# Optimization experiments

Hardware: AMD Instinct MI355X
Metric: run time of the kernel (lower is better)

The kernel has to match this reference:

```python
import jax, jax.numpy as jnp
import numpy as np


def setup_inputs() -> dict:
    key = jax.random.key(0)
    k1, k2 = jax.random.split(key)
    B, M, L, C, F, K = 8, 32, 1024, 256, 256, 3
    x = jax.random.normal(k1, (B, M, L, C), dtype=jnp.float32)
    W = jax.random.normal(k2, (K, C, F), dtype=jnp.float32) * 0.02  # WIO layout
    b = jnp.zeros((F,), dtype=jnp.float32)
    return {"x": x, "W": W, "b": b}


def reference(x, W, b):
    # Original: tf.map_fn(Conv1D, x) over leading axis of [B, M, L, C].
    # Mathematically identical to one batched 'valid' Conv1D on [B*M, L, C].
    B, M, L, C = x.shape
    K, _, F = W.shape
    xf = x.reshape(B * M, L, C)
    y = jax.lax.conv_general_dilated(
        xf, W,
        window_strides=(1,),
        padding='VALID',
        dimension_numbers=('NWC', 'WIO', 'NWC'),
    ) + b
    return y.reshape(B, M, L - K + 1, F)
```

## Files before the change

### kernel.cpp

```cpp
#include <hip/hip_runtime.h>

typedef __attribute__((ext_vector_type(8))) short short8;
typedef __attribute__((ext_vector_type(4))) float f32x4;

constexpr int L = 1024, C = 256, F = 256;
constexpr int NIMG = 256;
constexpr int LOUT = 1022;
constexpr int KTOT = 768;
constexpr int BK = 32;
constexpr int NKI = KTOT / BK;
constexpr int LDT = 40;
constexpr long MAXROW = (long)NIMG * L - 1;

__device__ inline unsigned short f2bf(float f) {
  union { float f; unsigned u; } v; v.f = f;
  return (unsigned short)((v.u + 0x7FFFu + ((v.u >> 16) & 1u)) >> 16);
}

__device__ inline void g2l16(const unsigned short* g, unsigned short* l) {
  __builtin_amdgcn_global_load_lds(
      (const __attribute__((address_space(1))) unsigned int*)g,
      (__attribute__((address_space(3))) unsigned int*)l, 16, 0, 0);
}

__global__ void wprep(const float* __restrict__ W, unsigned short* __restrict__ Wt) {
  int tid = blockIdx.x * 256 + threadIdx.x;
  if (tid >= KTOT * F) return;
  int kc = tid >> 8, f = tid & 255;
  int kk = kc >> 5, kp = kc & 31;
  int fh = f >> 7,  np = f & 127;
  Wt[((size_t)(kk * 2 + fh) * 128 + np) * LDT + kp] = f2bf(W[tid]);
}

__global__ __launch_bounds__(256) void conv_mfma(
    const float* __restrict__ x, const unsigned short* __restrict__ Wt,
    const float* __restrict__ bias, float* __restrict__ y)
{
  __shared__ __align__(16) unsigned short As[128 * LDT];
  __shared__ __align__(16) unsigned short Bs[128 * LDT];

  const int bid = blockIdx.x;
  const int fh  = bid & 1;
  const int mt  = (bid >> 1) & 7;
  const int img = bid >> 4;
  const int l0  = mt * 128;

  const int tid  = threadIdx.x;
  const int lane = tid & 63;
  const int wv   = tid >> 6;
  const int wr   = wv >> 1;
  const int wc   = wv & 1;
  const int lr   = lane & 15;
  const int quad = lane >> 4;

  const int rbase = tid >> 3;
  const int c8    = tid & 7;

  f32x4 acc[4][4] = {};
  float4 av[4];

  auto load_A = [&](int kk) {
    const int k  = kk >> 3;
    const int c0 = (kk & 7) << 5;
    const long growb = (long)img * L + l0 + k + rbase;
#pragma unroll
    for (int j = 0; j < 4; ++j) {
      long gr = growb + j * 32;
      if (gr > MAXROW) gr = MAXROW;
      av[j] = *(const float4*)(x + gr * C + c0 + (c8 << 2));
    }
  };

  load_A(0);

  for (int kk = 0; kk < NKI; ++kk) {
    __syncthreads();
#pragma unroll
    for (int j = 0; j < 4; ++j) {
      const int row = rbase + j * 32;
      ushort4 w4;
      w4.x = f2bf(av[j].x); w4.y = f2bf(av[j].y);
      w4.z = f2bf(av[j].z); w4.w = f2bf(av[j].w);
      *(ushort4*)(As + row * LDT + (c8 << 2)) = w4;
    }
    {
      const unsigned short* bsrc = Wt + (size_t)(kk * 2 + fh) * 128 * LDT;
      g2l16(bsrc + (size_t)tid * 8,         Bs + (size_t)tid * 8);
      g2l16(bsrc + (size_t)(tid + 256) * 8, Bs + (size_t)(tid + 256) * 8);
      if (tid < 128)
        g2l16(bsrc + (size_t)(tid + 512) * 8, Bs + (size_t)(tid + 512) * 8);
    }
    __syncthreads();

    if (kk + 1 < NKI) load_A(kk + 1);

    short8 af[4], bf[4];
#pragma unroll
    for (int mi = 0; mi < 4; ++mi) {
      const int row = wr * 64 + mi * 16 + lr;
      af[mi] = *(const short8*)(As + row * LDT + quad * 8);
    }
#pragma unroll
    for (int ni = 0; ni < 4; ++ni) {
      const int nr = wc * 64 + ni * 16 + lr;
      bf[ni] = *(const short8*)(Bs + nr * LDT + quad * 8);
    }
#pragma unroll
    for (int mi = 0; mi < 4; ++mi)
#pragma unroll
      for (int ni = 0; ni < 4; ++ni)
        acc[mi][ni] = __builtin_amdgcn_mfma_f32_16x16x32_bf16(af[mi], bf[ni], acc[mi][ni], 0, 0, 0);
  }

  float bv[4];
#pragma unroll
  for (int ni = 0; ni < 4; ++ni)
    bv[ni] = bias[fh * 128 + wc * 64 + ni * 16 + lr];

#pragma unroll
  for (int mi = 0; mi < 4; ++mi) {
#pragma unroll
    for (int r = 0; r < 4; ++r) {
      const int lrow = l0 + wr * 64 + mi * 16 + quad * 4 + r;
      if (lrow < LOUT) {
        float* yp = y + ((size_t)img * LOUT + lrow) * F + fh * 128 + wc * 64 + lr;
#pragma unroll
        for (int ni = 0; ni < 4; ++ni)
          yp[ni * 16] = acc[mi][ni][r] + bv[ni];
      }
    }
  }
}

extern "C" void kernel_launch(void* const* d_in, const int* in_sizes, int n_in,
                              void* d_out, int out_size, void* d_ws, size_t ws_size,
                              hipStream_t stream) {
  const float* x = (const float*)d_in[0];
  const float* W = (const float*)d_in[1];
  const float* b = (const float*)d_in[2];
  float* y = (float*)d_out;
  unsigned short* Wt = (unsigned short*)d_ws;

  wprep<<<(KTOT * F + 255) / 256, 256, 0, stream>>>(W, Wt);
  conv_mfma<<<NIMG * 8 * 2, 256, 0, stream>>>(x, Wt, b, y);
}
```

Measured before the change: 576.9 us.

## Reuse one 130-row A slab across all three conv taps per channel slab

The loop is reordered to channel-slab outer and tap inner. One 130-row bf16 A tile is loaded and converted per 32-channel slab and reused for the three kernel taps by shifting the row offset, instead of being reloaded for every (tap, slab) pair. This cuts global x reads and fp32-to-bf16 conversions roughly threefold. It also drops the LDS row padding (stride 32 instead of 40), which may bring back bank conflicts on the short8 reads, and the weight layout is reordered to match.

```diff
diff --git a/kernel.cpp b/kernel.cpp
--- a/kernel.cpp
+++ b/kernel.cpp
@@ -6,10 +6,6 @@
 constexpr int L = 1024, C = 256, F = 256;
 constexpr int NIMG = 256;
 constexpr int LOUT = 1022;
-constexpr int KTOT = 768;
-constexpr int BK = 32;
-constexpr int NKI = KTOT / BK;
-constexpr int LDT = 40;
 constexpr long MAXROW = (long)NIMG * L - 1;
 
 __device__ inline unsigned short f2bf(float f) {
@@ -25,19 +21,19 @@
 
 __global__ void wprep(const float* __restrict__ W, unsigned short* __restrict__ Wt) {
   int tid = blockIdx.x * 256 + threadIdx.x;
-  if (tid >= KTOT * F) return;
   int kc = tid >> 8, f = tid & 255;
-  int kk = kc >> 5, kp = kc & 31;
-  int fh = f >> 7,  np = f & 127;
-  Wt[((size_t)(kk * 2 + fh) * 128 + np) * LDT + kp] = f2bf(W[tid]);
+  int k = kc >> 8, c = kc & 255;
+  int slab = c >> 5, kp = c & 31;
+  int fh = f >> 7, fp = f & 127;
+  Wt[(size_t)((((slab * 3 + k) * 2 + fh) * 128 + fp) * 32 + kp)] = f2bf(W[tid]);
 }
 
 __global__ __launch_bounds__(256) void conv_mfma(
     const float* __restrict__ x, const unsigned short* __restrict__ Wt,
     const float* __restrict__ bias, float* __restrict__ y)
 {
-  __shared__ __align__(16) unsigned short As[128 * LDT];
-  __shared__ __align__(16) unsigned short Bs[128 * LDT];
+  __shared__ __align__(16) unsigned short As[130 * 32];
+  __shared__ __align__(16) unsigned short Bs[128 * 32];
 
   const int bid = blockIdx.x;
   const int fh  = bid & 1;
@@ -53,63 +49,74 @@
   const int lr   = lane & 15;
   const int quad = lane >> 4;
 
-  const int rbase = tid >> 3;
-  const int c8    = tid & 7;
+  f32x4 acc[4][4] = {};
+  float4 av[2][2];
+  float4 avt[2];
 
-  f32x4 acc[4][4] = {};
-  float4 av[4];
+  const long gb  = (long)img * L + l0;
+  const int  qr  = tid >> 2;
+  const int  qc8 = (tid & 3) * 8;
 
-  auto load_A = [&](int kk) {
-    const int k  = kk >> 3;
-    const int c0 = (kk & 7) << 5;
-    const long growb = (long)img * L + l0 + k + rbase;
-#pragma unroll
-    for (int j = 0; j < 4; ++j) {
-      long gr = growb + j * 32;
-      if (gr > MAXROW) gr = MAXROW;
-      av[j] = *(const float4*)(x + gr * C + c0 + (c8 << 2));
+  auto issue_A = [&](int slab) {
+    const int cb = slab * 32;
+    long g0 = gb + qr;        if (g0 > MAXROW) g0 = MAXROW;
+    long g1 = gb + qr + 64;   if (g1 > MAXROW) g1 = MAXROW;
+    const float* p0 = x + g0 * C + cb + qc8;
+    const float* p1 = x + g1 * C + cb + qc8;
+    av[0][0] = *(const float4*)p0; av[0][1] = *(const float4*)(p0 + 4);
+    av[1][0] = *(const float4*)p1; av[1][1] = *(const float4*)(p1 + 4);
+    if (tid < 8) {
+      long g2 = gb + 128 + (tid >> 2); if (g2 > MAXROW) g2 = MAXROW;
+      const float* p2 = x + g2 * C + cb + (tid & 3) * 8;
+      avt[0] = *(const float4*)p2; avt[1] = *(const float4*)(p2 + 4);
     }
   };
 
-  load_A(0);
+  auto pack8 = [&](float4 a, float4 b) {
+    short8 r;
+    r[0] = (short)f2bf(a.x); r[1] = (short)f2bf(a.y);
+    r[2] = (short)f2bf(a.z); r[3] = (short)f2bf(a.w);
+    r[4] = (short)f2bf(b.x); r[5] = (short)f2bf(b.y);
+    r[6] = (short)f2bf(b.z); r[7] = (short)f2bf(b.w);
+    return r;
+  };
 
-  for (int kk = 0; kk < NKI; ++kk) {
-    __syncthreads();
+  auto write_A = [&]() {
+    *(short8*)(As + (size_t)tid * 8)         = pack8(av[0][0], av[0][1]);
+    *(short8*)(As + (size_t)(tid + 256) * 8) = pack8(av[1][0], av[1][1]);
+    if (tid < 8)
+      *(short8*)(As + (size_t)(512 + tid) * 8) = pack8(avt[0], avt[1]);
+  };
+
+  issue_A(0);
+
+  for (int slab = 0; slab < 8; ++slab) {
 #pragma unroll
-    for (int j = 0; j < 4; ++j) {
-      const int row = rbase + j * 32;
-      ushort4 w4;
-      w4.x = f2bf(av[j].x); w4.y = f2bf(av[j].y);
-      w4.z = f2bf(av[j].z); w4.w = f2bf(av[j].w);
-      *(ushort4*)(As + row * LDT + (c8 << 2)) = w4;
-    }
-    {
-      const unsigned short* bsrc = Wt + (size_t)(kk * 2 + fh) * 128 * LDT;
-      g2l16(bsrc + (size_t)tid * 8,         Bs + (size_t)tid * 8);
-      g2l16(bsrc + (size_t)(tid + 256) * 8, Bs + (size_t)(tid + 256) * 8);
-      if (tid < 128)
-        g2l16(bsrc + (size_t)(tid + 512) * 8, Bs + (size_t)(tid + 512) * 8);
-    }
-    __syncthreads();
+    for (int k = 0; k < 3; ++k) {
+      __syncthreads();
+      if (k == 0) write_A();
+      {
+        const unsigned short* bsrc = Wt + (size_t)((slab * 3 + k) * 2 + fh) * (128 * 32);
+        g2l16(bsrc + (size_t)tid * 8,         Bs + (size_t)tid * 8);
+        g2l16(bsrc + (size_t)(tid + 256) * 8, Bs + (size_t)(tid + 256) * 8);
+      }
+      __syncthreads();
 
-    if (kk + 1 < NKI) load_A(kk + 1);
+      if (k == 1 && slab < 7) issue_A(slab + 1);
 
-    short8 af[4], bf[4];
+      short8 af[4], bf[4];
 #pragma unroll
-    for (int mi = 0; mi < 4; ++mi) {
-      const int row = wr * 64 + mi * 16 + lr;
-      af[mi] = *(const short8*)(As + row * LDT + quad * 8);
-    }
-#pragma unroll
-    for (int ni = 0; ni < 4; ++ni) {
-      const int nr = wc * 64 + ni * 16 + lr;
-      bf[ni] = *(const short8*)(Bs + nr * LDT + quad * 8);
-    }
-#pragma unroll
-    for (int mi = 0; mi < 4; ++mi)
+      for (int mi = 0; mi < 4; ++mi)
+        af[mi] = *(const short8*)(As + (wr * 64 + mi * 16 + lr + k) * 32 + quad * 8);
 #pragma unroll
       for (int ni = 0; ni < 4; ++ni)
-        acc[mi][ni] = __builtin_amdgcn_mfma_f32_16x16x32_bf16(af[mi], bf[ni], acc[mi][ni], 0, 0, 0);
+        bf[ni] = *(const short8*)(Bs + (wc * 64 + ni * 16 + lr) * 32 + quad * 8);
+#pragma unroll
+      for (int mi = 0; mi < 4; ++mi)
+#pragma unroll
+        for (int ni = 0; ni < 4; ++ni)
+          acc[mi][ni] = __builtin_amdgcn_mfma_f32_16x16x32_bf16(af[mi], bf[ni], acc[mi][ni], 0, 0, 0);
+    }
   }
 
   float bv[4];
@@ -141,6 +148,6 @@
   float* y = (float*)d_out;
   unsigned short* Wt = (unsigned short*)d_ws;
 
-  wprep<<<(KTOT * F + 255) / 256, 256, 0, stream>>>(W, Wt);
+  wprep<<<768, 256, 0, stream>>>(W, Wt);
   conv_mfma<<<NIMG * 8 * 2, 256, 0, stream>>>(x, Wt, b, y);
 }
```

Result: faster. 523.7 us (-9.2%).
